# Kernel tuning notes

Measured on AMD Instinct MI355X. Metric: run time of the kernel, lower is better.

## Reference

```python
import jax, jax.numpy as jnp
import numpy as np

B, S, D = 32, 1024, 512
H = 8
DH = D // H  # 64
NEG = -1e32


def setup_inputs() -> dict:
    key = jax.random.key(0)
    k1, k2, k3, k4, k5 = jax.random.split(key, 5)
    return {
        "q": jax.random.normal(k1, (B, S, D), dtype=jnp.float32),
        "k": jax.random.normal(k2, (B, S, D), dtype=jnp.float32),
        "v1": jax.random.normal(k3, (B, S, D), dtype=jnp.float32),
        "v2": jax.random.normal(k4, (B, S, D), dtype=jnp.float32),
        "counter_attention_mask": jax.random.randint(k5, (B, S), 0, 2, dtype=jnp.int32),
    }


def _dual_attention(q, k, v1, v2, counter_attention_mask):
    b, s, d = q.shape
    # split heads: [b, h, s, dh]
    qh = q.reshape(b, s, H, DH).transpose(0, 2, 1, 3)
    kh = k.reshape(b, s, H, DH).transpose(0, 2, 1, 3)
    v1h = v1.reshape(b, s, H, DH).transpose(0, 2, 1, 3)
    v2h = v2.reshape(b, s, H, DH).transpose(0, 2, 1, 3)

    scale = 1.0 / jnp.sqrt(jnp.float32(DH))
    scores = jnp.einsum("bhqd,bhkd->bhqk", qh, kh) * scale  # [b,h,s,s]

    # create_mask(x, 0): allowed where triu(k=0)==0 -> strictly-causal (key < query)
    row = jnp.arange(s)
    causal = row[:, None] > row[None, :]  # [s, s], True = attend
    # counter mask: zero entries mask out those KEY positions
    counter = counter_attention_mask.astype(bool)[:, None, None, :]  # [b,1,1,s]
    allowed = causal[None, None, :, :] & counter

    scores = jnp.where(allowed, scores, NEG)
    attn = jax.nn.softmax(scores, axis=-1)  # dropout p=0 (eval) -> identity

    o1 = jnp.einsum("bhqk,bhkd->bhqd", attn, v1h)
    o2 = jnp.einsum("bhqk,bhkd->bhqd", attn, v2h)
    o1 = o1.transpose(0, 2, 1, 3).reshape(b, s, d)
    o2 = o2.transpose(0, 2, 1, 3).reshape(b, s, d)
    return o1, o2


def reference(q, k, v1, v2, counter_attention_mask):
    return _dual_attention(q, k, v1, v2, counter_attention_mask)
```

## Files before the change

### kernel.cpp

```cpp
#include <hip/hip_runtime.h>
#include <hip/hip_bf16.h>

#define B_ 32
#define S_ 1024
#define D_ 512
#define H_ 8
#define DH_ 64
#define QBLK 64
#define KVB 32
#define NWAVE 4
#define NBLK 2048
#define NEGF (-1e30f)
#define THR 8.0f

using f32x4 = __attribute__((ext_vector_type(4))) float;
using bf16x8 = __attribute__((ext_vector_type(8))) short;
using bf16x4 = __attribute__((ext_vector_type(4))) short;

__device__ __forceinline__ unsigned int cvt_pk_bf16(float lo, float hi) {
  unsigned int r;
  asm("v_cvt_pk_bf16_f32 %0, %1, %2" : "=v"(r) : "v"(lo), "v"(hi));
  return r;
}

__device__ __forceinline__ f32x4 mfma16(bf16x8 a, bf16x8 b, f32x4 c) {
  return __builtin_amdgcn_mfma_f32_16x16x32_bf16(a, b, c, 0, 0, 0);
}

__device__ __forceinline__ int swz(int r) { return ((r ^ (r >> 3)) & 7) << 3; }
__device__ __forceinline__ int swzV(int r) { return ((r ^ (r >> 3)) & 7) << 2; }

__global__ __launch_bounds__(256, 3) void attn_kernel(
    const float* __restrict__ qg, const float* __restrict__ kg,
    const float* __restrict__ v1g, const float* __restrict__ v2g,
    const int* __restrict__ cmask, float* __restrict__ out) {
  const int wg = ((int)blockIdx.x & 7) * (NBLK / 8) + ((int)blockIdx.x >> 3);
  const int j = wg & 7;
  const int h = (wg >> 3) & 7;
  const int b = wg >> 6;
  const int tid = threadIdx.x;
  const int wid = tid >> 6;
  const int lane = tid & 63;
  const int l15 = lane & 15;
  const int lg = lane >> 4;

  __shared__ alignas(16) unsigned short sK[2][KVB * 64];
  __shared__ alignas(16) unsigned short sV1[2][64 * KVB];
  __shared__ alignas(16) unsigned short sV2[2][64 * KVB];
  __shared__ unsigned int sMaskW[32];

  const float SCL = 0.125f * 1.44269504089f;

  const float* qgb = qg + (size_t)b * S_ * D_ + h * DH_;
  const float* kgb = kg + (size_t)b * S_ * D_ + h * DH_;
  const float* v1b = v1g + (size_t)b * S_ * D_ + h * DH_;
  const float* v2b = v2g + (size_t)b * S_ * D_ + h * DH_;
  const int cmb = b * S_;

#pragma unroll
  for (int c = 0; c < 4; ++c) {
    const int chunk = wid * 4 + c;
    const int cm = cmask[cmb + chunk * 64 + lane];
    const unsigned long long bm = __ballot(cm != 0);
    if (lane == 0) {
      sMaskW[2 * chunk] = (unsigned int)bm;
      sMaskW[2 * chunk + 1] = (unsigned int)(bm >> 32);
    }
  }

  const int skv = tid >> 3;
  const int sd0 = (tid & 7) * 8;
  const int sKoff = skv * 64 + (sd0 ^ swz(skv));
  const unsigned int oK = (unsigned)skv * D_ + sd0;
  const int kvE = (tid >> 4) * 2;
  const int dq = (tid & 15) * 4;
  const unsigned int oV = (unsigned)kvE * D_ + dq;

  float4 rK0, rK1, rV1a, rV1b, rV2a, rV2b;
  auto issue = [&](int kv0) {
    const float* p = kgb + (oK + (unsigned)kv0 * D_);
    rK0 = *reinterpret_cast<const float4*>(p);
    rK1 = *reinterpret_cast<const float4*>(p + 4);
    const float* pv1 = v1b + (oV + (unsigned)kv0 * D_);
    const float* pv2 = v2b + (oV + (unsigned)kv0 * D_);
    rV1a = *reinterpret_cast<const float4*>(pv1);
    rV1b = *reinterpret_cast<const float4*>(pv1 + D_);
    rV2a = *reinterpret_cast<const float4*>(pv2);
    rV2b = *reinterpret_cast<const float4*>(pv2 + D_);
  };

  auto stage_write = [&](int buf) {
    bf16x8 kw;
    reinterpret_cast<unsigned int*>(&kw)[0] = cvt_pk_bf16(rK0.x, rK0.y);
    reinterpret_cast<unsigned int*>(&kw)[1] = cvt_pk_bf16(rK0.z, rK0.w);
    reinterpret_cast<unsigned int*>(&kw)[2] = cvt_pk_bf16(rK1.x, rK1.y);
    reinterpret_cast<unsigned int*>(&kw)[3] = cvt_pk_bf16(rK1.z, rK1.w);
    *reinterpret_cast<bf16x8*>(&sK[buf][sKoff]) = kw;
    const float* a1 = reinterpret_cast<const float*>(&rV1a);
    const float* b1 = reinterpret_cast<const float*>(&rV1b);
    const float* a2 = reinterpret_cast<const float*>(&rV2a);
    const float* b2 = reinterpret_cast<const float*>(&rV2b);
#pragma unroll
    for (int e = 0; e < 4; ++e) {
      const int d = dq + e;
      const int off = d * KVB + (kvE ^ swzV(d));
      *reinterpret_cast<unsigned int*>(&sV1[buf][off]) = cvt_pk_bf16(a1[e], b1[e]);
      *reinterpret_cast<unsigned int*>(&sV2[buf][off]) = cvt_pk_bf16(a2[e], b2[e]);
    }
  };

  float* outB = out + (size_t)B_ * S_ * D_;

  auto run_qblock = [&](int qb) {
    const int qt = qb * QBLK;
    const int qrow = qt + wid * 16 + l15;

    bf16x8 qf[2];
    {
      const float* qp = qgb + (unsigned)qrow * D_;
#pragma unroll
      for (int jk = 0; jk < 2; ++jk) {
        float4 a = *reinterpret_cast<const float4*>(qp + jk * 32 + lg * 8);
        float4 c = *reinterpret_cast<const float4*>(qp + jk * 32 + lg * 8 + 4);
        bf16x8 q8;
        reinterpret_cast<unsigned int*>(&q8)[0] = cvt_pk_bf16(a.x * SCL, a.y * SCL);
        reinterpret_cast<unsigned int*>(&q8)[1] = cvt_pk_bf16(a.z * SCL, a.w * SCL);
        reinterpret_cast<unsigned int*>(&q8)[2] = cvt_pk_bf16(c.x * SCL, c.y * SCL);
        reinterpret_cast<unsigned int*>(&q8)[3] = cvt_pk_bf16(c.z * SCL, c.w * SCL);
        qf[jk] = q8;
      }
    }

    f32x4 o1[4], o2[4];
    float m_ = NEGF, l_ = 0.f;
#pragma unroll
    for (int i = 0; i < 4; ++i) {
      o1[i] = f32x4{0.f, 0.f, 0.f, 0.f};
      o2[i] = f32x4{0.f, 0.f, 0.f, 0.f};
    }

    const int ntile = 2 * qb + 2;
    issue(0);
    for (int ti = 0; ti < ntile; ++ti) {
      const int kv0 = ti * KVB;
      const int buf = ti & 1;
      stage_write(buf);
      if (ti + 1 < ntile) issue(kv0 + KVB);
      asm volatile("s_waitcnt lgkmcnt(0)" ::: "memory");
      __builtin_amdgcn_s_barrier();
      __builtin_amdgcn_sched_barrier(0);

      if (kv0 <= qt + wid * 16 + 14) {
        f32x4 sa[2];
#pragma unroll
        for (int nb = 0; nb < 2; ++nb) {
          sa[nb] = f32x4{0.f, 0.f, 0.f, 0.f};
          const int key = nb * 16 + l15;
#pragma unroll
          for (int jk = 0; jk < 2; ++jk) {
            bf16x8 kf = *reinterpret_cast<const bf16x8*>(
                &sK[buf][key * 64 + ((jk * 32 + lg * 8) ^ swz(key))]);
            sa[nb] = mfma16(kf, qf[jk], sa[nb]);
          }
        }
        const unsigned int bits = sMaskW[ti];
        int thr = qrow - kv0;
        thr = thr < 0 ? 0 : (thr > KVB ? KVB : thr);
        const unsigned int allow =
            bits & ((thr >= 32) ? 0xFFFFFFFFu : ((1u << thr) - 1u));
        float pmax = NEGF;
#pragma unroll
        for (int nb = 0; nb < 2; ++nb) {
          const unsigned int sub = (allow >> (nb * 16 + lg * 4)) & 0xFu;
#pragma unroll
          for (int r = 0; r < 4; ++r) {
            const float s = (sub & (1u << r)) ? sa[nb][r] : NEGF;
            sa[nb][r] = s;
            pmax = fmaxf(pmax, s);
          }
        }
        if (__any(pmax > m_ + THR)) {
          float mx = fmaxf(pmax, __shfl_xor(pmax, 16));
          mx = fmaxf(mx, __shfl_xor(mx, 32));
          const float mnew = fmaxf(m_, mx);
          const float fac = exp2f(m_ - mnew);
          l_ *= fac;
          m_ = mnew;
#pragma unroll
          for (int nd = 0; nd < 4; ++nd) { o1[nd] *= fac; o2[nd] *= fac; }
        }
        float rs = 0.f;
#pragma unroll
        for (int nb = 0; nb < 2; ++nb)
#pragma unroll
          for (int r = 0; r < 4; ++r) {
            const float p = exp2f(sa[nb][r] - m_);
            sa[nb][r] = p;
            rs += p;
          }
        l_ += rs;

        bf16x8 pb;
        reinterpret_cast<unsigned int*>(&pb)[0] = cvt_pk_bf16(sa[0][0], sa[0][1]);
        reinterpret_cast<unsigned int*>(&pb)[1] = cvt_pk_bf16(sa[0][2], sa[0][3]);
        reinterpret_cast<unsigned int*>(&pb)[2] = cvt_pk_bf16(sa[1][0], sa[1][1]);
        reinterpret_cast<unsigned int*>(&pb)[3] = cvt_pk_bf16(sa[1][2], sa[1][3]);

#pragma unroll
        for (int nd = 0; nd < 4; ++nd) {
          const int drow = nd * 16 + l15;
          const int swd = swzV(drow);
          const int rbase = drow * KVB;
          const int kvA = (lg * 4) ^ swd;
          const int kvB = (16 + lg * 4) ^ swd;
          bf16x8 v1f, v2f;
          *reinterpret_cast<bf16x4*>(&v1f) =
              *reinterpret_cast<const bf16x4*>(&sV1[buf][rbase + kvA]);
          *reinterpret_cast<bf16x4*>(reinterpret_cast<short*>(&v1f) + 4) =
              *reinterpret_cast<const bf16x4*>(&sV1[buf][rbase + kvB]);
          *reinterpret_cast<bf16x4*>(&v2f) =
              *reinterpret_cast<const bf16x4*>(&sV2[buf][rbase + kvA]);
          *reinterpret_cast<bf16x4*>(reinterpret_cast<short*>(&v2f) + 4) =
              *reinterpret_cast<const bf16x4*>(&sV2[buf][rbase + kvB]);
          o1[nd] = mfma16(v1f, pb, o1[nd]);
          o2[nd] = mfma16(v2f, pb, o2[nd]);
        }
      }
    }

    float lsum = l_;
    lsum += __shfl_xor(lsum, 16);
    lsum += __shfl_xor(lsum, 32);

    const bool deg = (m_ <= -9.9e29f);
    float* cb = reinterpret_cast<float*>(&sK[0][0]);
    const int blockDeg = __syncthreads_or(deg ? 1 : 0);
    if (blockDeg) {
      const int d = tid & 63;
      const int sg = tid >> 6;
      float c1 = 0.f, c2 = 0.f;
      const float* p1 = v1b + d;
      const float* p2 = v2b + d;
#pragma unroll 4
      for (int s = sg; s < S_; s += 4) {
        c1 += p1[(unsigned)s * D_];
        c2 += p2[(unsigned)s * D_];
      }
      cb[sg * 64 + d] = c1;
      cb[256 + sg * 64 + d] = c2;
      __syncthreads();
      if (tid < 64) {
        float t1 = 0.f, t2 = 0.f;
#pragma unroll
        for (int g = 0; g < 4; ++g) {
          t1 += cb[g * 64 + tid];
          t2 += cb[256 + g * 64 + tid];
        }
        cb[512 + tid] = t1;
        cb[576 + tid] = t2;
      }
      __syncthreads();
    }

    const float invl = deg ? (1.0f / (float)S_) : (1.0f / lsum);
    const size_t rbase = ((size_t)b * S_ + qrow) * D_ + h * DH_;
#pragma unroll
    for (int nd = 0; nd < 4; ++nd) {
      const int d0 = nd * 16 + lg * 4;
      float4 cs1 = {0.f, 0.f, 0.f, 0.f}, cs2 = {0.f, 0.f, 0.f, 0.f};
      if (blockDeg) {
        cs1 = *reinterpret_cast<const float4*>(&cb[512 + d0]);
        cs2 = *reinterpret_cast<const float4*>(&cb[576 + d0]);
      }
      float4 w1, w2;
      w1.x = (deg ? cs1.x : o1[nd][0]) * invl;
      w1.y = (deg ? cs1.y : o1[nd][1]) * invl;
      w1.z = (deg ? cs1.z : o1[nd][2]) * invl;
      w1.w = (deg ? cs1.w : o1[nd][3]) * invl;
      w2.x = (deg ? cs2.x : o2[nd][0]) * invl;
      w2.y = (deg ? cs2.y : o2[nd][1]) * invl;
      w2.z = (deg ? cs2.z : o2[nd][2]) * invl;
      w2.w = (deg ? cs2.w : o2[nd][3]) * invl;
      *reinterpret_cast<float4*>(&out[rbase + d0]) = w1;
      *reinterpret_cast<float4*>(&outB[rbase + d0]) = w2;
    }
    __syncthreads();
  };

  run_qblock(15 - j);
  run_qblock(j);
}

extern "C" void kernel_launch(void* const* d_in, const int* in_sizes, int n_in,
                              void* d_out, int out_size, void* d_ws, size_t ws_size,
                              hipStream_t stream) {
  const float* q = (const float*)d_in[0];
  const float* k = (const float*)d_in[1];
  const float* v1 = (const float*)d_in[2];
  const float* v2 = (const float*)d_in[3];
  const int* cm = (const int*)d_in[4];
  float* out = (float*)d_out;

  attn_kernel<<<dim3(NBLK), dim3(256), 0, stream>>>(q, k, v1, v2, cm, out);
}
```

Before: 213.8 us.

## Process a contiguous 128-row query block per workgroup sharing each K/V tile

Each workgroup now handles one 128-row query block: every wave holds two 16-row query groups with separate softmax state and accumulators, and both consume each staged K/V tile. Before, each workgroup ran two separate 64-row passes (a late block and an early block), each streaming its own K/V prefix. The change aims to halve the K/V loads and bf16 conversions per query row. In exchange, register pressure roughly doubles for accumulators, and workloads become unbalanced across workgroups because the causal length now varies from 4 to 32 tiles instead of being paired to a constant total.

```diff
diff --git a/kernel.cpp b/kernel.cpp
--- a/kernel.cpp
+++ b/kernel.cpp
@@ -6,9 +6,8 @@
 #define D_ 512
 #define H_ 8
 #define DH_ 64
-#define QBLK 64
+#define QBLK 128
 #define KVB 32
-#define NWAVE 4
 #define NBLK 2048
 #define NEGF (-1e30f)
 #define THR 8.0f
@@ -35,14 +34,15 @@
     const float* __restrict__ v1g, const float* __restrict__ v2g,
     const int* __restrict__ cmask, float* __restrict__ out) {
   const int wg = ((int)blockIdx.x & 7) * (NBLK / 8) + ((int)blockIdx.x >> 3);
-  const int j = wg & 7;
+  const int qb = 7 - (wg & 7);
   const int h = (wg >> 3) & 7;
   const int b = wg >> 6;
+  const int qt = qb * QBLK;
   const int tid = threadIdx.x;
   const int wid = tid >> 6;
   const int lane = tid & 63;
   const int l15 = lane & 15;
-  const int lg = lane >> 4;
+  const int lgr = lane >> 4;
 
   __shared__ alignas(16) unsigned short sK[2][KVB * 64];
   __shared__ alignas(16) unsigned short sV1[2][64 * KVB];
@@ -50,6 +50,8 @@
   __shared__ unsigned int sMaskW[32];
 
   const float SCL = 0.125f * 1.44269504089f;
+  const int qrow0 = qt + wid * 16 + l15;
+  const int qrow1 = qrow0 + 64;
 
   const float* qgb = qg + (size_t)b * S_ * D_ + h * DH_;
   const float* kgb = kg + (size_t)b * S_ * D_ + h * DH_;
@@ -66,6 +68,26 @@
       sMaskW[2 * chunk] = (unsigned int)bm;
       sMaskW[2 * chunk + 1] = (unsigned int)(bm >> 32);
     }
+  }
+
+  bf16x8 qf0[2], qf1[2];
+  {
+    auto loadQ = [&](int qrow, bf16x8 (&qf)[2]) {
+      const float* qp = qgb + (unsigned)qrow * D_;
+#pragma unroll
+      for (int jk = 0; jk < 2; ++jk) {
+        float4 a = *reinterpret_cast<const float4*>(qp + jk * 32 + lgr * 8);
+        float4 c = *reinterpret_cast<const float4*>(qp + jk * 32 + lgr * 8 + 4);
+        bf16x8 q8;
+        reinterpret_cast<unsigned int*>(&q8)[0] = cvt_pk_bf16(a.x * SCL, a.y * SCL);
+        reinterpret_cast<unsigned int*>(&q8)[1] = cvt_pk_bf16(a.z * SCL, a.w * SCL);
+        reinterpret_cast<unsigned int*>(&q8)[2] = cvt_pk_bf16(c.x * SCL, c.y * SCL);
+        reinterpret_cast<unsigned int*>(&q8)[3] = cvt_pk_bf16(c.z * SCL, c.w * SCL);
+        qf[jk] = q8;
+      }
+    };
+    loadQ(qrow0, qf0);
+    loadQ(qrow1, qf1);
   }
 
   const int skv = tid >> 3;
@@ -109,164 +131,155 @@
     }
   };
 
+  f32x4 o1a[4], o2a[4], o1b[4], o2b[4];
+  float m0 = NEGF, l0 = 0.f, m1 = NEGF, l1 = 0.f;
+#pragma unroll
+  for (int i = 0; i < 4; ++i) {
+    o1a[i] = f32x4{0.f, 0.f, 0.f, 0.f};
+    o2a[i] = f32x4{0.f, 0.f, 0.f, 0.f};
+    o1b[i] = f32x4{0.f, 0.f, 0.f, 0.f};
+    o2b[i] = f32x4{0.f, 0.f, 0.f, 0.f};
+  }
+
+  auto group_tile = [&](int buf, int ti, int kv0, int qrow,
+                        bf16x8 (&qf)[2], float& m_, float& l_,
+                        f32x4 (&o1)[4], f32x4 (&o2)[4]) {
+    f32x4 sa[2];
+#pragma unroll
+    for (int nb = 0; nb < 2; ++nb) {
+      sa[nb] = f32x4{0.f, 0.f, 0.f, 0.f};
+      const int key = nb * 16 + l15;
+#pragma unroll
+      for (int jk = 0; jk < 2; ++jk) {
+        bf16x8 kf = *reinterpret_cast<const bf16x8*>(
+            &sK[buf][key * 64 + ((jk * 32 + lgr * 8) ^ swz(key))]);
+        sa[nb] = mfma16(kf, qf[jk], sa[nb]);
+      }
+    }
+    const unsigned int bits = sMaskW[ti];
+    int thr = qrow - kv0;
+    thr = thr < 0 ? 0 : (thr > KVB ? KVB : thr);
+    const unsigned int allow =
+        bits & ((thr >= 32) ? 0xFFFFFFFFu : ((1u << thr) - 1u));
+    float pmax = NEGF;
+#pragma unroll
+    for (int nb = 0; nb < 2; ++nb) {
+      const unsigned int sub = (allow >> (nb * 16 + lgr * 4)) & 0xFu;
+#pragma unroll
+      for (int r = 0; r < 4; ++r) {
+        const float s = (sub & (1u << r)) ? sa[nb][r] : NEGF;
+        sa[nb][r] = s;
+        pmax = fmaxf(pmax, s);
+      }
+    }
+    if (__any(pmax > m_ + THR)) {
+      float mx = fmaxf(pmax, __shfl_xor(pmax, 16));
+      mx = fmaxf(mx, __shfl_xor(mx, 32));
+      const float mnew = fmaxf(m_, mx);
+      const float fac = exp2f(m_ - mnew);
+      l_ *= fac;
+      m_ = mnew;
+#pragma unroll
+      for (int nd = 0; nd < 4; ++nd) { o1[nd] *= fac; o2[nd] *= fac; }
+    }
+    float rs = 0.f;
+#pragma unroll
+    for (int nb = 0; nb < 2; ++nb)
+#pragma unroll
+      for (int r = 0; r < 4; ++r) {
+        const float p = exp2f(sa[nb][r] - m_);
+        sa[nb][r] = p;
+        rs += p;
+      }
+    l_ += rs;
+    bf16x8 pb;
+    reinterpret_cast<unsigned int*>(&pb)[0] = cvt_pk_bf16(sa[0][0], sa[0][1]);
+    reinterpret_cast<unsigned int*>(&pb)[1] = cvt_pk_bf16(sa[0][2], sa[0][3]);
+    reinterpret_cast<unsigned int*>(&pb)[2] = cvt_pk_bf16(sa[1][0], sa[1][1]);
+    reinterpret_cast<unsigned int*>(&pb)[3] = cvt_pk_bf16(sa[1][2], sa[1][3]);
+#pragma unroll
+    for (int nd = 0; nd < 4; ++nd) {
+      const int drow = nd * 16 + l15;
+      const int swd = swzV(drow);
+      const int rbase = drow * KVB;
+      const int kvA = (lgr * 4) ^ swd;
+      const int kvB = (16 + lgr * 4) ^ swd;
+      bf16x8 v1f, v2f;
+      *reinterpret_cast<bf16x4*>(&v1f) =
+          *reinterpret_cast<const bf16x4*>(&sV1[buf][rbase + kvA]);
+      *reinterpret_cast<bf16x4*>(reinterpret_cast<short*>(&v1f) + 4) =
+          *reinterpret_cast<const bf16x4*>(&sV1[buf][rbase + kvB]);
+      *reinterpret_cast<bf16x4*>(&v2f) =
+          *reinterpret_cast<const bf16x4*>(&sV2[buf][rbase + kvA]);
+      *reinterpret_cast<bf16x4*>(reinterpret_cast<short*>(&v2f) + 4) =
+          *reinterpret_cast<const bf16x4*>(&sV2[buf][rbase + kvB]);
+      o1[nd] = mfma16(v1f, pb, o1[nd]);
+      o2[nd] = mfma16(v2f, pb, o2[nd]);
+    }
+  };
+
+  const int ntile = 4 * qb + 4;
+  issue(0);
+  for (int ti = 0; ti < ntile; ++ti) {
+    const int kv0 = ti * KVB;
+    const int buf = ti & 1;
+    stage_write(buf);
+    if (ti + 1 < ntile) issue(kv0 + KVB);
+    asm volatile("s_waitcnt lgkmcnt(0)" ::: "memory");
+    __builtin_amdgcn_s_barrier();
+    __builtin_amdgcn_sched_barrier(0);
+
+    if (kv0 <= qt + 64 + wid * 16 + 14)
+      group_tile(buf, ti, kv0, qrow1, qf1, m1, l1, o1b, o2b);
+    if (kv0 <= qt + wid * 16 + 14)
+      group_tile(buf, ti, kv0, qrow0, qf0, m0, l0, o1a, o2a);
+  }
+
+  float ls0 = l0, ls1 = l1;
+  ls0 += __shfl_xor(ls0, 16);
+  ls0 += __shfl_xor(ls0, 32);
+  ls1 += __shfl_xor(ls1, 16);
+  ls1 += __shfl_xor(ls1, 32);
+
+  const bool deg0 = (m0 <= -9.9e29f);
+  const bool deg1 = (m1 <= -9.9e29f);
+  float* cb = reinterpret_cast<float*>(&sK[0][0]);
+  const int blockDeg = __syncthreads_or((deg0 || deg1) ? 1 : 0);
+  if (blockDeg) {
+    const int d = tid & 63;
+    const int sg = tid >> 6;
+    float c1 = 0.f, c2 = 0.f;
+    const float* p1 = v1b + d;
+    const float* p2 = v2b + d;
+#pragma unroll 4
+    for (int s = sg; s < S_; s += 4) {
+      c1 += p1[(unsigned)s * D_];
+      c2 += p2[(unsigned)s * D_];
+    }
+    cb[sg * 64 + d] = c1;
+    cb[256 + sg * 64 + d] = c2;
+    __syncthreads();
+    if (tid < 64) {
+      float t1 = 0.f, t2 = 0.f;
+#pragma unroll
+      for (int g = 0; g < 4; ++g) {
+        t1 += cb[g * 64 + tid];
+        t2 += cb[256 + g * 64 + tid];
+      }
+      cb[512 + tid] = t1;
+      cb[576 + tid] = t2;
+    }
+    __syncthreads();
+  }
+
   float* outB = out + (size_t)B_ * S_ * D_;
-
-  auto run_qblock = [&](int qb) {
-    const int qt = qb * QBLK;
-    const int qrow = qt + wid * 16 + l15;
-
-    bf16x8 qf[2];
-    {
-      const float* qp = qgb + (unsigned)qrow * D_;
-#pragma unroll
-      for (int jk = 0; jk < 2; ++jk) {
-        float4 a = *reinterpret_cast<const float4*>(qp + jk * 32 + lg * 8);
-        float4 c = *reinterpret_cast<const float4*>(qp + jk * 32 + lg * 8 + 4);
-        bf16x8 q8;
-        reinterpret_cast<unsigned int*>(&q8)[0] = cvt_pk_bf16(a.x * SCL, a.y * SCL);
-        reinterpret_cast<unsigned int*>(&q8)[1] = cvt_pk_bf16(a.z * SCL, a.w * SCL);
-        reinterpret_cast<unsigned int*>(&q8)[2] = cvt_pk_bf16(c.x * SCL, c.y * SCL);
-        reinterpret_cast<unsigned int*>(&q8)[3] = cvt_pk_bf16(c.z * SCL, c.w * SCL);
-        qf[jk] = q8;
-      }
-    }
-
-    f32x4 o1[4], o2[4];
-    float m_ = NEGF, l_ = 0.f;
-#pragma unroll
-    for (int i = 0; i < 4; ++i) {
-      o1[i] = f32x4{0.f, 0.f, 0.f, 0.f};
-      o2[i] = f32x4{0.f, 0.f, 0.f, 0.f};
-    }
-
-    const int ntile = 2 * qb + 2;
-    issue(0);
-    for (int ti = 0; ti < ntile; ++ti) {
-      const int kv0 = ti * KVB;
-      const int buf = ti & 1;
-      stage_write(buf);
-      if (ti + 1 < ntile) issue(kv0 + KVB);
-      asm volatile("s_waitcnt lgkmcnt(0)" ::: "memory");
-      __builtin_amdgcn_s_barrier();
-      __builtin_amdgcn_sched_barrier(0);
-
-      if (kv0 <= qt + wid * 16 + 14) {
-        f32x4 sa[2];
-#pragma unroll
-        for (int nb = 0; nb < 2; ++nb) {
-          sa[nb] = f32x4{0.f, 0.f, 0.f, 0.f};
-          const int key = nb * 16 + l15;
-#pragma unroll
-          for (int jk = 0; jk < 2; ++jk) {
-            bf16x8 kf = *reinterpret_cast<const bf16x8*>(
-                &sK[buf][key * 64 + ((jk * 32 + lg * 8) ^ swz(key))]);
-            sa[nb] = mfma16(kf, qf[jk], sa[nb]);
-          }
-        }
-        const unsigned int bits = sMaskW[ti];
-        int thr = qrow - kv0;
-        thr = thr < 0 ? 0 : (thr > KVB ? KVB : thr);
-        const unsigned int allow =
-            bits & ((thr >= 32) ? 0xFFFFFFFFu : ((1u << thr) - 1u));
-        float pmax = NEGF;
-#pragma unroll
-        for (int nb = 0; nb < 2; ++nb) {
-          const unsigned int sub = (allow >> (nb * 16 + lg * 4)) & 0xFu;
-#pragma unroll
-          for (int r = 0; r < 4; ++r) {
-            const float s = (sub & (1u << r)) ? sa[nb][r] : NEGF;
-            sa[nb][r] = s;
-            pmax = fmaxf(pmax, s);
-          }
-        }
-        if (__any(pmax > m_ + THR)) {
-          float mx = fmaxf(pmax, __shfl_xor(pmax, 16));
-          mx = fmaxf(mx, __shfl_xor(mx, 32));
-          const float mnew = fmaxf(m_, mx);
-          const float fac = exp2f(m_ - mnew);
-          l_ *= fac;
-          m_ = mnew;
-#pragma unroll
-          for (int nd = 0; nd < 4; ++nd) { o1[nd] *= fac; o2[nd] *= fac; }
-        }
-        float rs = 0.f;
-#pragma unroll
-        for (int nb = 0; nb < 2; ++nb)
-#pragma unroll
-          for (int r = 0; r < 4; ++r) {
-            const float p = exp2f(sa[nb][r] - m_);
-            sa[nb][r] = p;
-            rs += p;
-          }
-        l_ += rs;
-
-        bf16x8 pb;
-        reinterpret_cast<unsigned int*>(&pb)[0] = cvt_pk_bf16(sa[0][0], sa[0][1]);
-        reinterpret_cast<unsigned int*>(&pb)[1] = cvt_pk_bf16(sa[0][2], sa[0][3]);
-        reinterpret_cast<unsigned int*>(&pb)[2] = cvt_pk_bf16(sa[1][0], sa[1][1]);
-        reinterpret_cast<unsigned int*>(&pb)[3] = cvt_pk_bf16(sa[1][2], sa[1][3]);
-
-#pragma unroll
-        for (int nd = 0; nd < 4; ++nd) {
-          const int drow = nd * 16 + l15;
-          const int swd = swzV(drow);
-          const int rbase = drow * KVB;
-          const int kvA = (lg * 4) ^ swd;
-          const int kvB = (16 + lg * 4) ^ swd;
-          bf16x8 v1f, v2f;
-          *reinterpret_cast<bf16x4*>(&v1f) =
-              *reinterpret_cast<const bf16x4*>(&sV1[buf][rbase + kvA]);
-          *reinterpret_cast<bf16x4*>(reinterpret_cast<short*>(&v1f) + 4) =
-              *reinterpret_cast<const bf16x4*>(&sV1[buf][rbase + kvB]);
-          *reinterpret_cast<bf16x4*>(&v2f) =
-              *reinterpret_cast<const bf16x4*>(&sV2[buf][rbase + kvA]);
-          *reinterpret_cast<bf16x4*>(reinterpret_cast<short*>(&v2f) + 4) =
-              *reinterpret_cast<const bf16x4*>(&sV2[buf][rbase + kvB]);
-          o1[nd] = mfma16(v1f, pb, o1[nd]);
-          o2[nd] = mfma16(v2f, pb, o2[nd]);
-        }
-      }
-    }
-
-    float lsum = l_;
-    lsum += __shfl_xor(lsum, 16);
-    lsum += __shfl_xor(lsum, 32);
-
-    const bool deg = (m_ <= -9.9e29f);
-    float* cb = reinterpret_cast<float*>(&sK[0][0]);
-    const int blockDeg = __syncthreads_or(deg ? 1 : 0);
-    if (blockDeg) {
-      const int d = tid & 63;
-      const int sg = tid >> 6;
-      float c1 = 0.f, c2 = 0.f;
-      const float* p1 = v1b + d;
-      const float* p2 = v2b + d;
-#pragma unroll 4
-      for (int s = sg; s < S_; s += 4) {
-        c1 += p1[(unsigned)s * D_];
-        c2 += p2[(unsigned)s * D_];
-      }
-      cb[sg * 64 + d] = c1;
-      cb[256 + sg * 64 + d] = c2;
-      __syncthreads();
-      if (tid < 64) {
-        float t1 = 0.f, t2 = 0.f;
-#pragma unroll
-        for (int g = 0; g < 4; ++g) {
-          t1 += cb[g * 64 + tid];
-          t2 += cb[256 + g * 64 + tid];
-        }
-        cb[512 + tid] = t1;
-        cb[576 + tid] = t2;
-      }
-      __syncthreads();
-    }
-
+  auto storeG = [&](int qrow, bool deg, float lsum,
+                    f32x4 (&o1)[4], f32x4 (&o2)[4]) {
     const float invl = deg ? (1.0f / (float)S_) : (1.0f / lsum);
     const size_t rbase = ((size_t)b * S_ + qrow) * D_ + h * DH_;
 #pragma unroll
     for (int nd = 0; nd < 4; ++nd) {
-      const int d0 = nd * 16 + lg * 4;
+      const int d0 = nd * 16 + lgr * 4;
       float4 cs1 = {0.f, 0.f, 0.f, 0.f}, cs2 = {0.f, 0.f, 0.f, 0.f};
       if (blockDeg) {
         cs1 = *reinterpret_cast<const float4*>(&cb[512 + d0]);
@@ -284,11 +297,9 @@
       *reinterpret_cast<float4*>(&out[rbase + d0]) = w1;
       *reinterpret_cast<float4*>(&outB[rbase + d0]) = w2;
     }
-    __syncthreads();
   };
-
-  run_qblock(15 - j);
-  run_qblock(j);
+  storeG(qrow0, deg0, ls0, o1a, o2a);
+  storeG(qrow1, deg1, ls1, o1b, o2b);
 }
 
 extern "C" void kernel_launch(void* const* d_in, const int* in_sizes, int n_in,
```

New measurement: 220.5 us. +3.1%, slower.
